# Optimization experiments

Measured on AMD Instinct MI355X. Metric: run time of the kernel, lower is better.

The kernel has to match this reference:

```python
import jax, jax.numpy as jnp
import numpy as np

K = 4  # spline order (degree K-1)


def bspline_basis(x, t, k):
    """Evaluate the k nonzero B-spline basis functions of order k at x.

    x: [B, I] floats; t: [G+2k-1] clamped knot vector.
    Returns (idx [B,I,k] int32 basis indices, basis [B,I,k] values),
    using the de Boor / NURBS-book triangular recursion (vectorized over B,I;
    Python loops only over the small fixed order k).
    """
    m = t.shape[0]
    # interval index: t[i] <= x < t[i+1], clamped to valid span [k-1, m-k-1]
    i = jnp.clip(jnp.searchsorted(t, x, side='right') - 1, k - 1, m - k - 1)
    p = k - 1
    N = [jnp.ones_like(x)]
    left, right = [], []
    for j in range(1, p + 1):
        left.append(x - t[i + 1 - j])
        right.append(t[i + j] - x)
        saved = jnp.zeros_like(x)
        Nn = []
        for r in range(j):
            temp = N[r] / (right[r] + left[j - 1 - r])
            Nn.append(saved + right[r] * temp)
            saved = left[j - 1 - r] * temp
        Nn.append(saved)
        N = Nn
    idx = jnp.stack([i - p + j for j in range(k)], axis=-1)   # [B,I,k]
    basis = jnp.stack(N, axis=-1)                             # [B,I,k]
    return idx, basis


def setup_inputs() -> dict:
    key = jax.random.key(0)
    k1, k2 = jax.random.split(key)
    B, I, O, G, k = 2048, 128, 128, 64, K
    t0, t1 = -1.0, 1.0
    x = jax.random.uniform(k1, (B, I), jnp.float32, minval=t0, maxval=t1)
    # xavier_normal_ for fan_in=in_dim, fan_out=out_dim (per-slice heuristic)
    std = (2.0 / (I + O)) ** 0.5
    w = jax.random.normal(k2, (G + k, I, O), jnp.float32) * std
    t = jnp.concatenate([
        jnp.full((k - 1,), t0, jnp.float32),
        jnp.linspace(t0, t1, G + 1, dtype=jnp.float32),
        jnp.full((k - 1,), t1, jnp.float32),
    ])
    return {"x": x, "w": w, "t": t}


def reference(x, w, t):
    k = K
    B, I = x.shape
    O = w.shape[2]
    idx, basis = bspline_basis(x, t, k)                       # [B,I,k]
    # activation slot uses the last row of w (torch index -1)
    act_idx = jnp.full((B, I, 1), w.shape[0] - 1, idx.dtype)
    idx_full = jnp.concatenate([idx, act_idx], axis=-1)       # [B,I,k+1]
    y = jnp.concatenate([basis, jax.nn.silu(x)[..., None]], axis=-1)  # [B,I,k+1]
    wt = jnp.transpose(w, (1, 0, 2))                          # [I, G+k, O]
    w2 = wt[jnp.arange(I)[None, :, None], idx_full]           # [B,I,k+1,O] gather
    return jnp.einsum('bij,bijo->bo', y, w2)                  # [B,O]
```

## Files before the change

kernel.cpp:

```cpp
#include <hip/hip_runtime.h>
#include <math.h>

#define B_TOTAL 2048
#define I_DIM   128
#define O_DIM   128
#define GK      68
#define NKNOT   71
#define BT      64
#define BTILES  (B_TOTAL / BT)
#define RI      8
#define NR      (I_DIM / RI)
#define THREADS 512
#define SLICE_FLOATS (GK * O_DIM)
#define CHUNKS  (SLICE_FLOATS / 256)
#define WS_NEED ((size_t)NR * B_TOTAL * O_DIM * 4)

__device__ __forceinline__ float rdlanef(float v, int l) {
    return __int_as_float(__builtin_amdgcn_readlane(__float_as_int(v), l));
}

template<bool USE_WS>
__global__ __launch_bounds__(THREADS, 4)
void flashkan_main(const float* __restrict__ x,
                   const float* __restrict__ w,
                   const float* __restrict__ t,
                   float* __restrict__ dst) {
    __shared__ float wbuf[2][SLICE_FLOATS];
    __shared__ float t_sh[NKNOT];

    const int tid  = threadIdx.x;
    const int bid  = blockIdx.x;
    const int bt   = bid >> 4;
    const int r    = bid & 15;
    const int b0   = bt * BT;
    const int i0   = r * RI;
    const int wave = tid >> 6;
    const int lane = tid & 63;
    const int h    = lane >> 5;
    const int l32  = lane & 31;

    if (tid < NKNOT) t_sh[tid] = t[tid];
    __syncthreads();

    float cf0, cf1, cf2, cf3, cf4;
    int   cg;
    {
        const int bl = lane >> 3;
        const int ii = lane & 7;
        const float xv = x[(size_t)(b0 + wave * 8 + bl) * I_DIM + (i0 + ii)];

        int ik = 3 + (int)floorf((xv + 1.0f) * 32.0f);
        ik = min(max(ik, 3), 66);
        while (ik < 66 && xv >= t_sh[ik + 1]) ++ik;
        while (ik > 3 && xv < t_sh[ik]) --ik;

        float l0, l1, l2, r0, r1, r2;
        float N0 = 1.0f, N1, N2, N3;
        l0 = xv - t_sh[ik];
        r0 = t_sh[ik + 1] - xv;
        {
            float temp = N0 / (r0 + l0);
            N0 = r0 * temp;
            N1 = l0 * temp;
        }
        l1 = xv - t_sh[ik - 1];
        r1 = t_sh[ik + 2] - xv;
        {
            float saved = 0.0f, temp;
            temp = N0 / (r0 + l1);
            N0 = saved + r0 * temp;
            saved = l1 * temp;
            temp = N1 / (r1 + l0);
            N1 = saved + r1 * temp;
            N2 = l0 * temp;
        }
        l2 = xv - t_sh[ik - 2];
        r2 = t_sh[ik + 3] - xv;
        {
            float saved = 0.0f, temp;
            temp = N0 / (r0 + l2);
            N0 = saved + r0 * temp;
            saved = l2 * temp;
            temp = N1 / (r1 + l1);
            N1 = saved + r1 * temp;
            saved = l1 * temp;
            temp = N2 / (r2 + l0);
            N2 = saved + r2 * temp;
            N3 = l0 * temp;
        }
        cf0 = N0; cf1 = N1; cf2 = N2; cf3 = N3;
        cf4 = xv / (1.0f + expf(-xv));
        cg  = ik - 3;
    }

    auto stage = [&](int sel, int i_abs) {
        for (int c = wave; c < CHUNKS; c += 8) {
            const int f = c * 256 + lane * 4;
            const int g = f >> 7;
            const int o = f & (O_DIM - 1);
            const float* src = w + ((size_t)g * I_DIM + i_abs) * O_DIM + o;
            void* dstp = (void*)&wbuf[sel][c * 256];
            __builtin_amdgcn_global_load_lds(
                (const __attribute__((address_space(1))) void*)src,
                (__attribute__((address_space(3))) void*)dstp,
                16, 0, 0);
        }
    };

    float4 acc[8];
    #pragma unroll
    for (int bl = 0; bl < 8; ++bl) acc[bl] = make_float4(0.f, 0.f, 0.f, 0.f);

    auto compute = [&](int ii, const float* buf) {
        const float4 sv = ((const float4*)(buf + 67 * O_DIM))[l32];
        #pragma unroll
        for (int bl = 0; bl < 8; ++bl) {
            const int srcl = (bl << 3) | ii;
            const float c0 = rdlanef(cf0, srcl);
            const float c1 = rdlanef(cf1, srcl);
            const float c2 = rdlanef(cf2, srcl);
            const float c3 = rdlanef(cf3, srcl);
            const float c4 = rdlanef(cf4, srcl);
            const int   g0 = __builtin_amdgcn_readlane(cg, srcl);

            const float cA  = h ? c1 : c0;
            const float cB  = h ? c3 : c2;
            const float c4h = h ? 0.0f : c4;

            const float4* rp = (const float4*)(buf + (size_t)(g0 + h) * O_DIM) + l32;
            const float4 vA = rp[0];
            const float4 vB = rp[64];

            float4& a = acc[bl];
            a.x += cA * vA.x + cB * vB.x + c4h * sv.x;
            a.y += cA * vA.y + cB * vB.y + c4h * sv.y;
            a.z += cA * vA.z + cB * vB.z + c4h * sv.z;
            a.w += cA * vA.w + cB * vB.w + c4h * sv.w;
        }
    };

    stage(0, i0);
    __syncthreads();

    for (int iib = 0; iib < RI; iib += 2) {
        stage(1, i0 + iib + 1);
        compute(iib, wbuf[0]);
        __syncthreads();
        if (iib + 2 < RI) stage(0, i0 + iib + 2);
        compute(iib + 1, wbuf[1]);
        __syncthreads();
    }

    #pragma unroll
    for (int bl = 0; bl < 8; ++bl) {
        float4 a = acc[bl];
        a.x += __shfl(a.x, lane ^ 32);
        a.y += __shfl(a.y, lane ^ 32);
        a.z += __shfl(a.z, lane ^ 32);
        a.w += __shfl(a.w, lane ^ 32);
        const int b = b0 + wave * 8 + bl;
        if (lane < 32) {
            if (USE_WS) {
                float4* dp = (float4*)(dst + ((size_t)r * B_TOTAL + b) * O_DIM) + l32;
                *dp = a;
            } else {
                float* dp = dst + (size_t)b * O_DIM + l32 * 4;
                atomicAdd(dp,     a.x);
                atomicAdd(dp + 1, a.y);
                atomicAdd(dp + 2, a.z);
                atomicAdd(dp + 3, a.w);
            }
        }
    }
}

__global__ __launch_bounds__(256)
void flashkan_reduce(const float* __restrict__ ws, float* __restrict__ out) {
    const int f = blockIdx.x * 256 + threadIdx.x;
    const float4* base = (const float4*)ws + f;
    float4 s = make_float4(0.0f, 0.0f, 0.0f, 0.0f);
    #pragma unroll
    for (int r2 = 0; r2 < NR; ++r2) {
        const float4 v = base[(size_t)r2 * (B_TOTAL * O_DIM / 4)];
        s.x += v.x; s.y += v.y; s.z += v.z; s.w += v.w;
    }
    ((float4*)out)[f] = s;
}

extern "C" void kernel_launch(void* const* d_in, const int* in_sizes, int n_in,
                              void* d_out, int out_size, void* d_ws, size_t ws_size,
                              hipStream_t stream) {
    const float* x = (const float*)d_in[0];
    const float* w = (const float*)d_in[1];
    const float* t = (const float*)d_in[2];
    float* out = (float*)d_out;

    dim3 grid(BTILES * NR);
    dim3 block(THREADS);

    if (ws_size >= WS_NEED) {
        float* ws = (float*)d_ws;
        flashkan_main<true><<<grid, block, 0, stream>>>(x, w, t, ws);
        flashkan_reduce<<<B_TOTAL * O_DIM / 4 / 256, 256, 0, stream>>>(ws, out);
    } else {
        hipMemsetAsync(out, 0, (size_t)out_size * sizeof(float), stream);
        flashkan_main<false><<<grid, block, 0, stream>>>(x, w, t, out);
    }
}
```

Baseline: 38.62 us.

## Convert weights to fp16 and use packed half2 FMAs in main kernel

Adds a pre-pass that converts the fp32 weights into fp16 in the workspace. The main kernel now stages half-precision slices into LDS, halving LDS footprint and load traffic. Its inner loop is restructured so each half-wave handles a different batch row and accumulates with packed half2 FMAs over all four basis terms plus silu, which also removes the final cross-half shuffle reduction. It adds an extra conversion kernel that reads all of w every call, and it reduces accuracy through fp16 coefficients and fp16 partial sums.

```diff
diff --git a/kernel.cpp b/kernel.cpp
--- a/kernel.cpp
+++ b/kernel.cpp
@@ -1,4 +1,5 @@
 #include <hip/hip_runtime.h>
+#include <hip/hip_fp16.h>
 #include <math.h>
 
 #define B_TOTAL 2048
@@ -11,21 +12,34 @@
 #define RI      8
 #define NR      (I_DIM / RI)
 #define THREADS 512
-#define SLICE_FLOATS (GK * O_DIM)
-#define CHUNKS  (SLICE_FLOATS / 256)
-#define WS_NEED ((size_t)NR * B_TOTAL * O_DIM * 4)
-
-__device__ __forceinline__ float rdlanef(float v, int l) {
-    return __int_as_float(__builtin_amdgcn_readlane(__float_as_int(v), l));
+#define SLICE_ELEMS (GK * O_DIM)
+#define CHUNKS  (SLICE_ELEMS * 2 / 1024)
+#define W_ELEMS ((size_t)GK * I_DIM * O_DIM)
+#define PART_FLOATS ((size_t)NR * B_TOTAL * O_DIM)
+#define WS_FULL (PART_FLOATS * 4 + W_ELEMS * 2)
+#define WS_MIN  (W_ELEMS * 2)
+
+__device__ __forceinline__ __half2 u2h2(unsigned u) {
+    return __builtin_bit_cast(__half2, u);
+}
+
+__global__ __launch_bounds__(256)
+void wcvt(const float* __restrict__ w, __half* __restrict__ wh) {
+    const int e4 = blockIdx.x * 256 + threadIdx.x;
+    const float4 v = ((const float4*)w)[e4];
+    uint2 o;
+    o.x = __builtin_bit_cast(unsigned, __floats2half2_rn(v.x, v.y));
+    o.y = __builtin_bit_cast(unsigned, __floats2half2_rn(v.z, v.w));
+    ((uint2*)wh)[e4] = o;
 }
 
 template<bool USE_WS>
 __global__ __launch_bounds__(THREADS, 4)
 void flashkan_main(const float* __restrict__ x,
-                   const float* __restrict__ w,
+                   const __half* __restrict__ wh,
                    const float* __restrict__ t,
                    float* __restrict__ dst) {
-    __shared__ float wbuf[2][SLICE_FLOATS];
+    __shared__ __align__(16) __half wbuf[2][SLICE_ELEMS];
     __shared__ float t_sh[NKNOT];
 
     const int tid  = threadIdx.x;
@@ -42,8 +56,8 @@
     if (tid < NKNOT) t_sh[tid] = t[tid];
     __syncthreads();
 
-    float cf0, cf1, cf2, cf3, cf4;
-    int   cg;
+    unsigned cp0, cp1, cp2, cp3, cp4;
+    int cg;
     {
         const int bl = lane >> 3;
         const int ii = lane & 7;
@@ -88,18 +102,23 @@
             N2 = saved + r2 * temp;
             N3 = l0 * temp;
         }
-        cf0 = N0; cf1 = N1; cf2 = N2; cf3 = N3;
-        cf4 = xv / (1.0f + expf(-xv));
+        const float silu = xv / (1.0f + expf(-xv));
+
+        cp0 = 0x00010001u * (unsigned)__half_as_ushort(__float2half_rn(N0));
+        cp1 = 0x00010001u * (unsigned)__half_as_ushort(__float2half_rn(N1));
+        cp2 = 0x00010001u * (unsigned)__half_as_ushort(__float2half_rn(N2));
+        cp3 = 0x00010001u * (unsigned)__half_as_ushort(__float2half_rn(N3));
+        cp4 = 0x00010001u * (unsigned)__half_as_ushort(__float2half_rn(silu));
         cg  = ik - 3;
     }
 
     auto stage = [&](int sel, int i_abs) {
         for (int c = wave; c < CHUNKS; c += 8) {
-            const int f = c * 256 + lane * 4;
-            const int g = f >> 7;
-            const int o = f & (O_DIM - 1);
-            const float* src = w + ((size_t)g * I_DIM + i_abs) * O_DIM + o;
-            void* dstp = (void*)&wbuf[sel][c * 256];
+            const int e = c * 512 + lane * 8;
+            const int g = e >> 7;
+            const int o = e & (O_DIM - 1);
+            const __half* src = wh + ((size_t)g * I_DIM + i_abs) * O_DIM + o;
+            void* dstp = (void*)((char*)&wbuf[sel][0] + c * 1024);
             __builtin_amdgcn_global_load_lds(
                 (const __attribute__((address_space(1))) void*)src,
                 (__attribute__((address_space(3))) void*)dstp,
@@ -107,35 +126,56 @@
         }
     };
 
-    float4 acc[8];
+    float4  acc32[4];
     #pragma unroll
-    for (int bl = 0; bl < 8; ++bl) acc[bl] = make_float4(0.f, 0.f, 0.f, 0.f);
-
-    auto compute = [&](int ii, const float* buf) {
-        const float4 sv = ((const float4*)(buf + 67 * O_DIM))[l32];
+    for (int gi = 0; gi < 4; ++gi) acc32[gi] = make_float4(0.f, 0.f, 0.f, 0.f);
+
+    auto compute = [&](int ii, const __half* buf) {
+        const char* bufc = (const char*)buf;
+        const uint2 su = *(const uint2*)(bufc + 67 * 256 + l32 * 8);
+        const __half2 sv0 = u2h2(su.x), sv1 = u2h2(su.y);
         #pragma unroll
-        for (int bl = 0; bl < 8; ++bl) {
-            const int srcl = (bl << 3) | ii;
-            const float c0 = rdlanef(cf0, srcl);
-            const float c1 = rdlanef(cf1, srcl);
-            const float c2 = rdlanef(cf2, srcl);
-            const float c3 = rdlanef(cf3, srcl);
-            const float c4 = rdlanef(cf4, srcl);
-            const int   g0 = __builtin_amdgcn_readlane(cg, srcl);
-
-            const float cA  = h ? c1 : c0;
-            const float cB  = h ? c3 : c2;
-            const float c4h = h ? 0.0f : c4;
-
-            const float4* rp = (const float4*)(buf + (size_t)(g0 + h) * O_DIM) + l32;
-            const float4 vA = rp[0];
-            const float4 vB = rp[64];
-
-            float4& a = acc[bl];
-            a.x += cA * vA.x + cB * vB.x + c4h * sv.x;
-            a.y += cA * vA.y + cB * vB.y + c4h * sv.y;
-            a.z += cA * vA.z + cB * vB.z + c4h * sv.z;
-            a.w += cA * vA.w + cB * vB.w + c4h * sv.w;
+        for (int gi = 0; gi < 4; ++gi) {
+            const int sl0 = ((gi * 2    ) << 3) | ii;
+            const int sl1 = ((gi * 2 + 1) << 3) | ii;
+            const unsigned c0 = h ? __builtin_amdgcn_readlane(cp0, sl1)
+                                  : __builtin_amdgcn_readlane(cp0, sl0);
+            const unsigned c1 = h ? __builtin_amdgcn_readlane(cp1, sl1)
+                                  : __builtin_amdgcn_readlane(cp1, sl0);
+            const unsigned c2 = h ? __builtin_amdgcn_readlane(cp2, sl1)
+                                  : __builtin_amdgcn_readlane(cp2, sl0);
+            const unsigned c3 = h ? __builtin_amdgcn_readlane(cp3, sl1)
+                                  : __builtin_amdgcn_readlane(cp3, sl0);
+            const unsigned c4 = h ? __builtin_amdgcn_readlane(cp4, sl1)
+                                  : __builtin_amdgcn_readlane(cp4, sl0);
+            const int      g0 = h ? __builtin_amdgcn_readlane(cg, sl1)
+                                  : __builtin_amdgcn_readlane(cg, sl0);
+
+            const char* rp = bufc + g0 * 256 + l32 * 8;
+            const uint2 r0 = *(const uint2*)(rp);
+            const uint2 r1 = *(const uint2*)(rp + 256);
+            const uint2 r2 = *(const uint2*)(rp + 512);
+            const uint2 r3 = *(const uint2*)(rp + 768);
+
+            __half2 a0 = __half2(__float2half_rn(0.f), __float2half_rn(0.f));
+            __half2 a1 = a0;
+            a0 = __hfma2(u2h2(c0), u2h2(r0.x), a0);
+            a1 = __hfma2(u2h2(c0), u2h2(r0.y), a1);
+            a0 = __hfma2(u2h2(c1), u2h2(r1.x), a0);
+            a1 = __hfma2(u2h2(c1), u2h2(r1.y), a1);
+            a0 = __hfma2(u2h2(c2), u2h2(r2.x), a0);
+            a1 = __hfma2(u2h2(c2), u2h2(r2.y), a1);
+            a0 = __hfma2(u2h2(c3), u2h2(r3.x), a0);
+            a1 = __hfma2(u2h2(c3), u2h2(r3.y), a1);
+            a0 = __hfma2(u2h2(c4), sv0, a0);
+            a1 = __hfma2(u2h2(c4), sv1, a1);
+
+            const float2 f0 = __half22float2(a0);
+            const float2 f1 = __half22float2(a1);
+            acc32[gi].x += f0.x;
+            acc32[gi].y += f0.y;
+            acc32[gi].z += f1.x;
+            acc32[gi].w += f1.y;
         }
     };
 
@@ -152,24 +192,18 @@
     }
 
     #pragma unroll
-    for (int bl = 0; bl < 8; ++bl) {
-        float4 a = acc[bl];
-        a.x += __shfl(a.x, lane ^ 32);
-        a.y += __shfl(a.y, lane ^ 32);
-        a.z += __shfl(a.z, lane ^ 32);
-        a.w += __shfl(a.w, lane ^ 32);
-        const int b = b0 + wave * 8 + bl;
-        if (lane < 32) {
-            if (USE_WS) {
-                float4* dp = (float4*)(dst + ((size_t)r * B_TOTAL + b) * O_DIM) + l32;
-                *dp = a;
-            } else {
-                float* dp = dst + (size_t)b * O_DIM + l32 * 4;
-                atomicAdd(dp,     a.x);
-                atomicAdd(dp + 1, a.y);
-                atomicAdd(dp + 2, a.z);
-                atomicAdd(dp + 3, a.w);
-            }
+    for (int gi = 0; gi < 4; ++gi) {
+        const int b = b0 + wave * 8 + gi * 2 + h;
+        const float4 a = acc32[gi];
+        if (USE_WS) {
+            float4* dp = (float4*)(dst + ((size_t)r * B_TOTAL + b) * O_DIM) + l32;
+            *dp = a;
+        } else {
+            float* dp = dst + (size_t)b * O_DIM + l32 * 4;
+            atomicAdd(dp,     a.x);
+            atomicAdd(dp + 1, a.y);
+            atomicAdd(dp + 2, a.z);
+            atomicAdd(dp + 3, a.w);
         }
     }
 }
@@ -197,13 +231,18 @@
 
     dim3 grid(BTILES * NR);
     dim3 block(THREADS);
-
-    if (ws_size >= WS_NEED) {
-        float* ws = (float*)d_ws;
-        flashkan_main<true><<<grid, block, 0, stream>>>(x, w, t, ws);
-        flashkan_reduce<<<B_TOTAL * O_DIM / 4 / 256, 256, 0, stream>>>(ws, out);
+    const int cvt_blocks = (int)(W_ELEMS / 4 / 256);
+
+    if (ws_size >= WS_FULL) {
+        float* part = (float*)d_ws;
+        __half* whp = (__half*)((char*)d_ws + PART_FLOATS * 4);
+        wcvt<<<cvt_blocks, 256, 0, stream>>>(w, whp);
+        flashkan_main<true><<<grid, block, 0, stream>>>(x, whp, t, part);
+        flashkan_reduce<<<B_TOTAL * O_DIM / 4 / 256, 256, 0, stream>>>(part, out);
     } else {
+        __half* whp = (__half*)d_ws;
         hipMemsetAsync(out, 0, (size_t)out_size * sizeof(float), stream);
-        flashkan_main<false><<<grid, block, 0, stream>>>(x, w, t, out);
-    }
-}
+        wcvt<<<cvt_blocks, 256, 0, stream>>>(w, whp);
+        flashkan_main<false><<<grid, block, 0, stream>>>(x, whp, t, out);
+    }
+}
```

New measurement: 43.39 us. 12.4% more time.
